# Performance work log

Hardware: AMD Instinct MI355X
Metric: run time of the kernel (lower is better)

## Reference

```python
import jax, jax.numpy as jnp
import numpy as np

D = 512
H = 2048
L = 8192
NSEG = 16
LN_EPS = 1e-6  # flax LayerNorm default


def _ln_tokens(x):
    # flax LayerNorm(reduction_axes=-2, feature_axes=-1, use_bias=False, use_scale=False):
    # mean/var reduced over the token axis (-2), per feature; no learned params.
    mu = jnp.mean(x, axis=-2, keepdims=True)
    var = jnp.var(x, axis=-2, keepdims=True)
    return (x - mu) * jax.lax.rsqrt(var + LN_EPS)


def setup_inputs() -> dict:
    key = jax.random.key(0)
    ks = jax.random.split(key, 8)
    xcat = jax.random.normal(ks[0], (L, D), dtype=jnp.float32)
    xsep = jnp.sort(jax.random.randint(ks[1], (L,), 0, NSEG)).astype(jnp.int64)
    s = 0.02
    Wqkv = jax.random.normal(ks[2], (D, 3 * D), dtype=jnp.float32) * s
    bqkv = jnp.zeros((3 * D,), dtype=jnp.float32)
    W1 = jax.random.normal(ks[3], (D, H), dtype=jnp.float32) * s
    b1 = jnp.zeros((H,), dtype=jnp.float32)
    W2 = jax.random.normal(ks[4], (H, D), dtype=jnp.float32) * s
    b2 = jnp.zeros((D,), dtype=jnp.float32)
    return {"xcat": xcat, "xsep": xsep, "Wqkv": Wqkv, "bqkv": bqkv,
            "W1": W1, "b1": b1, "W2": W2, "b2": b2}


def reference(xcat, xsep, Wqkv, bqkv, W1, b1, W2, b2):
    Ltok = xcat.shape[0]
    qkv = _ln_tokens(xcat) @ Wqkv + bqkv            # [L, 3D]
    q = qkv[:, :D]
    k = qkv[:, D:2 * D]
    # v = qkv[:, 2*D:3*D]  # computed in original but never used
    # unscaled scores; softmax FIRST, then mask, then renormalize (faithful to source)
    atten = jax.nn.softmax(jnp.einsum('id,jd->ij', q, k), axis=-1)  # [L, L]
    idx = jnp.arange(Ltok)
    mask = (xsep[None, :] == xsep[:, None]) & (idx[None, :] <= idx[:, None])
    atten = atten * mask
    atten = atten / (atten.sum(axis=-1, keepdims=True) + 1e-10)
    ctx = atten @ xcat                               # attention applied to raw xcat
    ffn = jax.nn.relu(_ln_tokens(ctx) @ W1 + b1) @ W2 + b2
    return (xcat + ffn, xsep)
```

## Files before the change

### kernel.cpp

```cpp
#include <hip/hip_runtime.h>
#include <math.h>

#define LTOK 8192
#define DDIM 512
#define HDIM 2048
#define NSEG 16
#define DCUT 64
#define ZROWS (NSEG * DCUT)
#define ZCH 64
#define NPART (ZCH * 4)
#define BM 128
#define BN 128
#define BK 64
#define PW 1280
#define PTILES (PW / BN)
#define ZGB (ZCH * (ZROWS / BM))
#define SPB (PTILES * 64)

typedef float f32x4 __attribute__((ext_vector_type(4)));
typedef short s16x8 __attribute__((ext_vector_type(8)));

static __device__ __forceinline__ short f2bf(float f) {
    union { float f; unsigned u; } v; v.f = f;
    unsigned r = (v.u + 0x7fffu + ((v.u >> 16) & 1u)) >> 16;
    return (short)r;
}
static __device__ __forceinline__ float bf2f(short s) {
    union { unsigned u; float f; } v;
    v.u = ((unsigned)(unsigned short)s) << 16;
    return v.f;
}

template<int GX, int GY>
__device__ __forceinline__ void swz_yslow(int& x, int& y) {
    constexpr int cpx = (GX * GY) >> 3;
    const int orig = blockIdx.y * GX + blockIdx.x;
    const int lg = (orig & 7) * cpx + (orig >> 3);
    y = lg / GX;
    x = lg - y * GX;
}

__global__ void ln_stats_partial(const float* __restrict__ X,
                                 float* __restrict__ psum, float* __restrict__ psumsq) {
    int c = threadIdx.x;
    int b = blockIdx.x;
    const float* p = X + (size_t)b * 256 * DDIM + c;
    float s = 0.f, s2 = 0.f;
    for (int r = 0; r < 256; ++r) {
        float v = p[(size_t)r * DDIM];
        s += v; s2 += v * v;
    }
    psum[b * DDIM + c] = s;
    psumsq[b * DDIM + c] = s2;
}

__global__ void ln_stats_final(const float* __restrict__ psum, const float* __restrict__ psumsq,
                               float* __restrict__ mu, float* __restrict__ rstd) {
    int c = threadIdx.x;
    float s = 0.f, s2 = 0.f;
    for (int b = 0; b < 32; ++b) { s += psum[b * DDIM + c]; s2 += psumsq[b * DDIM + c]; }
    float m = s / (float)LTOK;
    float var = s2 / (float)LTOK - m * m;
    mu[c] = m;
    rstd[c] = rsqrtf(var + 1e-6f);
}

__global__ void ln_apply_bf16(const float* __restrict__ X,
                              const float* __restrict__ mu, const float* __restrict__ rstd,
                              short* __restrict__ out) {
    int t = blockIdx.x * 256 + threadIdx.x;
    int base = t * 4;
    int c = base & (DDIM - 1);
    float4 v = *(const float4*)(X + base);
    short4 o;
    o.x = f2bf((v.x - mu[c + 0]) * rstd[c + 0]);
    o.y = f2bf((v.y - mu[c + 1]) * rstd[c + 1]);
    o.z = f2bf((v.z - mu[c + 2]) * rstd[c + 2]);
    o.w = f2bf((v.w - mu[c + 3]) * rstd[c + 3]);
    *(short4*)(out + base) = o;
}

__global__ void transpose_w(const float* __restrict__ W, int ldw, int n0,
                            short* __restrict__ WT, int R) {
    __shared__ short t[32][33];
    int nb = n0 + blockIdx.x * 32;
    int rb = blockIdx.y * 32;
    int tx = threadIdx.x & 31, ty = threadIdx.x >> 5;
    for (int rr = ty; rr < 32; rr += 8)
        t[rr][tx] = f2bf(W[(size_t)(rb + rr) * ldw + nb + tx]);
    __syncthreads();
    for (int rr = ty; rr < 32; rr += 8)
        WT[(size_t)(nb - n0 + rr) * R + rb + tx] = t[tx][rr];
}

__global__ void transpose_bf16(const float* __restrict__ X, short* __restrict__ XT) {
    __shared__ short t[32][33];
    int c0 = blockIdx.x * 32;
    int r0 = blockIdx.y * 32;
    int tx = threadIdx.x & 31, ty = threadIdx.x >> 5;
    for (int rr = ty; rr < 32; rr += 8)
        t[rr][tx] = f2bf(X[(size_t)(r0 + rr) * DDIM + c0 + tx]);
    __syncthreads();
    for (int rr = ty; rr < 32; rr += 8)
        XT[(size_t)(c0 + rr) * LTOK + r0 + tx] = t[tx][rr];
}

__global__ void seg_begin_k(const int* __restrict__ sep, int* __restrict__ begin,
                            float* __restrict__ out2) {
    int i = blockIdx.x * 256 + threadIdx.x;
    if (i < LTOK) {
        if (i == 0 || sep[i] != sep[i - 1]) begin[sep[i]] = i;
        out2[i] = (float)sep[i];
    }
}

__global__ void gather_qz(const short* __restrict__ qk, const int* __restrict__ sep,
                          const int* __restrict__ begin, short* __restrict__ qg) {
    const int gi = blockIdx.x;
    const int s = gi / DCUT, d = gi - s * DCUT;
    const int r = begin[s] + d;
    if ((unsigned)r < LTOK && sep[r] == s) {
        const short2* src = (const short2*)(qk + (size_t)r * 1024);
        short2* dst = (short2*)(qg + (size_t)gi * DDIM);
        dst[threadIdx.x] = src[threadIdx.x];
    }
}

__device__ __forceinline__ void stage_tile512(const short* __restrict__ src, int lda,
                                              short* lds, int tid) {
    const int wave = tid >> 6;
    const int lane = tid & 63;
    #pragma unroll
    for (int u = 0; u < 2; ++u) {
        const int c = u * 512 + wave * 64 + lane;
        const short* g = src + (size_t)(c >> 3) * lda + (c & 7) * 8;
        short* l = lds + (size_t)(u * 512 + wave * 64) * 8;
        __builtin_amdgcn_global_load_lds(
            (const __attribute__((address_space(1))) unsigned int*)g,
            (__attribute__((address_space(3))) unsigned int*)l,
            16, 0, 0);
    }
}

__device__ __forceinline__ void mma8_step(const short (*As)[BK], const short (*Bs)[BK],
                                          f32x4 acc[4][2], int wr, int wc, int grp, int lrow) {
    #pragma unroll
    for (int kk = 0; kk < 2; ++kk) {
        s16x8 af[4], bfr[2];
        #pragma unroll
        for (int f = 0; f < 4; ++f)
            af[f] = *(const s16x8*)&As[wr * 64 + f * 16 + lrow][grp * 8 + kk * 32];
        #pragma unroll
        for (int f = 0; f < 2; ++f)
            bfr[f] = *(const s16x8*)&Bs[wc * 32 + f * 16 + lrow][grp * 8 + kk * 32];
        #pragma unroll
        for (int fm = 0; fm < 4; ++fm)
            #pragma unroll
            for (int fn = 0; fn < 2; ++fn)
                acc[fm][fn] = __builtin_amdgcn_mfma_f32_16x16x32_bf16(
                    af[fm], bfr[fn], acc[fm][fn], 0, 0, 0);
    }
}

template<int EPI, int GX, int GY>
__global__ __launch_bounds__(512) void mm_bt8(const short* __restrict__ A, int lda,
        const short* __restrict__ BT, int ldb,
        const float* __restrict__ bias, const float* __restrict__ resid,
        float* __restrict__ Cf, short* __restrict__ Cb, int ldc, int K) {
    __shared__ short As[BM][BK];
    __shared__ short Bs[BN][BK];
    const int tid = threadIdx.x;
    const int wave = tid >> 6, lane = tid & 63, grp = lane >> 4, lrow = lane & 15;
    const int wr = wave >> 2, wc = wave & 3;
    int bx, by;
    swz_yslow<GX, GY>(bx, by);
    const int m0 = by * BM, n0 = bx * BN;
    if (EPI == 3) {
        A += (size_t)blockIdx.z * K;
        BT += (size_t)blockIdx.z * K;
    }
    f32x4 acc[4][2];
    #pragma unroll
    for (int a = 0; a < 4; ++a)
        #pragma unroll
        for (int b = 0; b < 2; ++b) acc[a][b] = (f32x4){0.f, 0.f, 0.f, 0.f};
    for (int k0 = 0; k0 < K; k0 += BK) {
        __syncthreads();
        stage_tile512(A + (size_t)m0 * lda + k0, lda, &As[0][0], tid);
        stage_tile512(BT + (size_t)n0 * ldb + k0, ldb, &Bs[0][0], tid);
        asm volatile("s_waitcnt vmcnt(0)" ::: "memory");
        __syncthreads();
        mma8_step(As, Bs, acc, wr, wc, grp, lrow);
    }
    #pragma unroll
    for (int fm = 0; fm < 4; ++fm) {
        #pragma unroll
        for (int i = 0; i < 4; ++i) {
            int row = m0 + wr * 64 + fm * 16 + grp * 4 + i;
            #pragma unroll
            for (int fn = 0; fn < 2; ++fn) {
                int col = n0 + wc * 32 + fn * 16 + lrow;
                float v = acc[fm][fn][i] + (EPI == 3 ? 0.f : bias[col]);
                if (EPI == 1) v = fmaxf(v, 0.f);
                if (EPI == 2) {
                    Cf[(size_t)row * ldc + col] = v + resid[(size_t)row * ldc + col];
                } else if (EPI == 3) {
                    Cb[(size_t)blockIdx.z * ((size_t)LTOK * ldc)
                       + (size_t)row * ldc + col] = f2bf(v);
                } else {
                    Cb[(size_t)row * ldc + col] = f2bf(v);
                }
            }
        }
    }
}

__global__ void ffn2_combine(const short* __restrict__ hp, const float* __restrict__ b2,
                             const float* __restrict__ xcat, float* __restrict__ out) {
    const int t = blockIdx.x * 256 + threadIdx.x;
    const int base = t * 4;
    const int c = base & (DDIM - 1);
    float4 r = *(const float4*)(xcat + base);
    float4 a;
    a.x = r.x + b2[c + 0];
    a.y = r.y + b2[c + 1];
    a.z = r.z + b2[c + 2];
    a.w = r.w + b2[c + 3];
    #pragma unroll
    for (int z = 0; z < 4; ++z) {
        short4 p = *(const short4*)(hp + (size_t)z * LTOK * DDIM + base);
        a.x += bf2f(p.x); a.y += bf2f(p.y); a.z += bf2f(p.z); a.w += bf2f(p.w);
    }
    *(float4*)(out + base) = a;
}

__global__ __launch_bounds__(512) void attn_zgsp(const short* __restrict__ qg,
        const short* __restrict__ qk,
        const int* __restrict__ sep, const int* __restrict__ begin,
        short* __restrict__ P, float* __restrict__ Zg) {
    __shared__ short As[BM][BK];
    __shared__ short Bs[BN][BK];
    const int tid = threadIdx.x;
    const int wave = tid >> 6, lane = tid & 63, grp = lane >> 4, lrow = lane & 15;
    const int wr = wave >> 2, wc = wave & 3;
    const int bid = blockIdx.x;
    const int grpi = bid / 9, rem = bid - grpi * 9;
    f32x4 acc[4][2];
    #pragma unroll
    for (int a = 0; a < 4; ++a)
        #pragma unroll
        for (int b = 0; b < 2; ++b) acc[a][b] = (f32x4){0.f, 0.f, 0.f, 0.f};

    if (rem < 4) {
        const int orig = grpi * 4 + rem;
        constexpr int cpx = ZGB >> 3;
        const int lg = (orig & 7) * cpx + (orig >> 3);
        const int bx = lg / (ZROWS / BM);
        const int by = lg - bx * (ZROWS / BM);
        const int g0 = by * BM;
        const int j0 = bx * BN;
        for (int k0 = 0; k0 < DDIM; k0 += BK) {
            __syncthreads();
            stage_tile512(qg + (size_t)g0 * DDIM + k0, DDIM, &As[0][0], tid);
            stage_tile512(qk + (size_t)j0 * 1024 + 512 + k0, 1024, &Bs[0][0], tid);
            asm volatile("s_waitcnt vmcnt(0)" ::: "memory");
            __syncthreads();
            mma8_step(As, Bs, acc, wr, wc, grp, lrow);
        }
        #pragma unroll
        for (int idx = 0; idx < 16; ++idx) {
            float z = __expf(acc[idx >> 2][0][idx & 3]) + __expf(acc[idx >> 2][1][idx & 3]);
            #pragma unroll
            for (int off = 1; off < 16; off <<= 1) z += __shfl_xor(z, off, 16);
            if (lrow == 0) {
                const int gi = g0 + wr * 64 + (idx >> 2) * 16 + grp * 4 + (idx & 3);
                Zg[(size_t)gi * NPART + bx * 4 + wc] = z;
            }
        }
    } else {
        const int orig = grpi * 5 + (rem - 4);
        constexpr int cpx = SPB >> 3;
        const int lg = (orig & 7) * cpx + (orig >> 3);
        const int by = lg / PTILES;
        const int bx = lg - by * PTILES;
        const int m0 = by * BM;
        const int jb0 = begin[sep[m0]] & ~(BN - 1);
        const int j0 = jb0 + bx * BN;
        if (j0 >= m0 + BM) return;
        for (int k0 = 0; k0 < DDIM; k0 += BK) {
            __syncthreads();
            stage_tile512(qk + (size_t)m0 * 1024 + k0, 1024, &As[0][0], tid);
            stage_tile512(qk + (size_t)j0 * 1024 + 512 + k0, 1024, &Bs[0][0], tid);
            asm volatile("s_waitcnt vmcnt(0)" ::: "memory");
            __syncthreads();
            mma8_step(As, Bs, acc, wr, wc, grp, lrow);
        }
        #pragma unroll
        for (int fm = 0; fm < 4; ++fm) {
            #pragma unroll
            for (int i = 0; i < 4; ++i) {
                const int row = m0 + wr * 64 + fm * 16 + grp * 4 + i;
                short* pr = P + (size_t)row * PW + (j0 - jb0) + wc * 32;
                #pragma unroll
                for (int fn = 0; fn < 2; ++fn)
                    pr[fn * 16 + lrow] = f2bf(__expf(acc[fm][fn][i]));
            }
        }
    }
}

__global__ void mask_inv(short* __restrict__ P,
                         const int* __restrict__ sep, const int* __restrict__ begin,
                         const float* __restrict__ Zg, float* __restrict__ invE) {
    const int wv = threadIdx.x >> 6, lane = threadIdx.x & 63;
    const int r = blockIdx.x * 4 + wv;
    const int m0 = r & ~(BM - 1);
    const int jb0 = begin[sep[m0]] & ~(BN - 1);
    const int kw = m0 + BM - jb0;
    const int sr = sep[r];
    const int jsr = begin[sr];
    short* Pr = P + (size_t)r * PW;
    float e = 0.f;
    for (int c = lane * 2; c < kw; c += 128) {
        short2 v = *(short2*)(Pr + c);
        const int col0 = jb0 + c;
        float p0 = bf2f(v.x), p1 = bf2f(v.y);
        if (col0 < jsr || col0 > r) { p0 = 0.f; v.x = 0; }
        if (col0 + 1 < jsr || col0 + 1 > r) { p1 = 0.f; v.y = 0; }
        e += p0 + p1;
        *(short2*)(Pr + c) = v;
    }
    const int d = r - jsr;
    float z = 0.f;
    if (d < DCUT) {
        const float* zr = Zg + (size_t)(sr * DCUT + d) * NPART;
        #pragma unroll
        for (int c = 0; c < NPART / 64; ++c) z += zr[c * 64 + lane];
    }
    #pragma unroll
    for (int off = 1; off < 64; off <<= 1) {
        e += __shfl_xor(e, off);
        z += __shfl_xor(z, off);
    }
    if (lane == 0) invE[r] = 1.f / (e + 1e-10f * z);
}

__global__ __launch_bounds__(512) void attn_pv(const short* __restrict__ P,
        const short* __restrict__ xbT,
        const int* __restrict__ sep, const int* __restrict__ begin,
        const float* __restrict__ invE, float* __restrict__ ctx) {
    __shared__ short As[BM][BK];
    __shared__ short Bs[BN][BK];
    const int tid = threadIdx.x;
    const int wave = tid >> 6, lane = tid & 63, grp = lane >> 4, lrow = lane & 15;
    const int wr = wave >> 2, wc = wave & 3;
    int bx, by;
    swz_yslow<4, 64>(bx, by);
    const int m0 = by * BM, n0 = bx * BN;
    const int jbase0 = begin[sep[m0]] & ~(BN - 1);
    const int kmax = m0 + BM - jbase0;
    f32x4 acc[4][2];
    #pragma unroll
    for (int a = 0; a < 4; ++a)
        #pragma unroll
        for (int b = 0; b < 2; ++b) acc[a][b] = (f32x4){0.f, 0.f, 0.f, 0.f};
    for (int k0 = 0; k0 < kmax; k0 += BK) {
        __syncthreads();
        stage_tile512(P + (size_t)m0 * PW + k0, PW, &As[0][0], tid);
        stage_tile512(xbT + (size_t)n0 * LTOK + jbase0 + k0, LTOK, &Bs[0][0], tid);
        asm volatile("s_waitcnt vmcnt(0)" ::: "memory");
        __syncthreads();
        mma8_step(As, Bs, acc, wr, wc, grp, lrow);
    }
    #pragma unroll
    for (int fm = 0; fm < 4; ++fm) {
        #pragma unroll
        for (int i = 0; i < 4; ++i) {
            int row = m0 + wr * 64 + fm * 16 + grp * 4 + i;
            float inv = invE[row];
            #pragma unroll
            for (int fn = 0; fn < 2; ++fn) {
                int col = n0 + wc * 32 + fn * 16 + lrow;
                ctx[(size_t)row * DDIM + col] = acc[fm][fn][i] * inv;
            }
        }
    }
}

extern "C" void kernel_launch(void* const* d_in, const int* in_sizes, int n_in,
                              void* d_out, int out_size, void* d_ws, size_t ws_size,
                              hipStream_t stream) {
    const float* xcat = (const float*)d_in[0];
    const int* sep = (const int*)d_in[1];
    const float* Wqkv = (const float*)d_in[2];
    const float* bqkv = (const float*)d_in[3];
    const float* W1 = (const float*)d_in[4];
    const float* b1 = (const float*)d_in[5];
    const float* W2 = (const float*)d_in[6];
    const float* b2 = (const float*)d_in[7];
    float* out = (float*)d_out;

    float* ws = (float*)d_ws;
    float* psum   = ws;
    float* psumsq = psum + 32 * DDIM;
    float* mu1    = psumsq + 32 * DDIM;
    float* rstd1  = mu1 + DDIM;
    float* mu2    = rstd1 + DDIM;
    float* rstd2  = mu2 + DDIM;
    float* invE   = rstd2 + DDIM;
    float* Zg     = invE + LTOK;
    int*   begin  = (int*)(Zg + (size_t)ZROWS * NPART);
    short* qg     = (short*)(begin + 1024);
    short* qk     = qg    + (size_t)ZROWS * DDIM;
    short* xbT    = qk    + (size_t)LTOK * 1024;
    short* lnx    = xbT   + (size_t)DDIM * LTOK;
    short* lnctx  = lnx   + (size_t)LTOK * DDIM;
    short* hb     = lnctx + (size_t)LTOK * DDIM;
    short* Pbuf   = hb;
    short* WqkvT  = hb    + (size_t)LTOK * HDIM;
    short* W1T    = WqkvT + (size_t)1024 * DDIM;
    short* W2T    = W1T   + (size_t)HDIM * DDIM;
    float* ctxF   = (float*)(W2T + (size_t)DDIM * HDIM);
    short* hpart  = qk;

    ln_stats_partial<<<dim3(32), dim3(512), 0, stream>>>(xcat, psum, psumsq);
    ln_stats_final<<<dim3(1), dim3(512), 0, stream>>>(psum, psumsq, mu1, rstd1);
    ln_apply_bf16<<<dim3(LTOK * DDIM / 4 / 256), dim3(256), 0, stream>>>(xcat, mu1, rstd1, lnx);

    transpose_w<<<dim3(32, 16), dim3(256), 0, stream>>>(Wqkv, 3 * DDIM, 0, WqkvT, DDIM);
    transpose_w<<<dim3(64, 16), dim3(256), 0, stream>>>(W1, HDIM, 0, W1T, DDIM);
    transpose_w<<<dim3(16, 64), dim3(256), 0, stream>>>(W2, DDIM, 0, W2T, HDIM);

    mm_bt8<0, 8, 64><<<dim3(8, 64), dim3(512), 0, stream>>>(
        lnx, DDIM, WqkvT, DDIM, bqkv, (const float*)nullptr,
        (float*)nullptr, qk, 1024, DDIM);

    seg_begin_k<<<dim3(32), dim3(256), 0, stream>>>(sep, begin, out + (size_t)LTOK * DDIM);
    transpose_bf16<<<dim3(16, 256), dim3(256), 0, stream>>>(xcat, xbT);

    gather_qz<<<dim3(ZROWS), dim3(256), 0, stream>>>(qk, sep, begin, qg);
    attn_zgsp<<<dim3(ZGB + SPB), dim3(512), 0, stream>>>(qg, qk, sep, begin, Pbuf, Zg);

    mask_inv<<<dim3(LTOK / 4), dim3(256), 0, stream>>>(Pbuf, sep, begin, Zg, invE);
    attn_pv<<<dim3(4, 64), dim3(512), 0, stream>>>(Pbuf, xbT, sep, begin, invE, ctxF);

    ln_stats_partial<<<dim3(32), dim3(512), 0, stream>>>(ctxF, psum, psumsq);
    ln_stats_final<<<dim3(1), dim3(512), 0, stream>>>(psum, psumsq, mu2, rstd2);
    ln_apply_bf16<<<dim3(LTOK * DDIM / 4 / 256), dim3(256), 0, stream>>>(ctxF, mu2, rstd2, lnctx);

    mm_bt8<1, 16, 64><<<dim3(16, 64), dim3(512), 0, stream>>>(
        lnctx, DDIM, W1T, DDIM, b1, (const float*)nullptr,
        (float*)nullptr, hb, HDIM, DDIM);

    mm_bt8<3, 4, 64><<<dim3(4, 64, 4), dim3(512), 0, stream>>>(
        hb, HDIM, W2T, HDIM, (const float*)nullptr, (const float*)nullptr,
        (float*)nullptr, hpart, DDIM, HDIM / 4);
    ffn2_combine<<<dim3(LTOK * DDIM / 4 / 256), dim3(256), 0, stream>>>(hpart, b2, xcat, out);
}
```

Measured before the change: 209.9 us.

## Fuse causal/segment mask into score epilogue and LN stats into PV epilogue

Applies the segment/causal mask directly when writing exp(scores) in attn_zgsp, so the row-sum pass becomes read-only instead of read-modify-write. Computes per-column sum and sum-of-squares of ctx in the attn_pv epilogue via shared-memory atomics and writes 64 partials, which removes a separate ln_stats_partial pass over ctx. Also halves DCUT, shrinking the Zg denominator-approximation work. The smaller DCUT changes how many near-diagonal rows get the tiny epsilon*Z correction, which may alter accuracy in edge cases.

New measurement: 216.9 us. +3.3%, slower.

```diff
diff --git a/kernel.cpp b/kernel.cpp
--- a/kernel.cpp
+++ b/kernel.cpp
@@ -5,7 +5,7 @@
 #define DDIM 512
 #define HDIM 2048
 #define NSEG 16
-#define DCUT 64
+#define DCUT 32
 #define ZROWS (NSEG * DCUT)
 #define ZCH 64
 #define NPART (ZCH * 4)
@@ -16,6 +16,9 @@
 #define PTILES (PW / BN)
 #define ZGB (ZCH * (ZROWS / BM))
 #define SPB (PTILES * 64)
+#define ZG_PER (ZGB / 128)
+#define SP_PER (SPB / 128)
+#define GRP_SZ (ZG_PER + SP_PER)
 
 typedef float f32x4 __attribute__((ext_vector_type(4)));
 typedef short s16x8 __attribute__((ext_vector_type(8)));
@@ -55,10 +58,10 @@
 }
 
 __global__ void ln_stats_final(const float* __restrict__ psum, const float* __restrict__ psumsq,
-                               float* __restrict__ mu, float* __restrict__ rstd) {
+                               float* __restrict__ mu, float* __restrict__ rstd, int nb) {
     int c = threadIdx.x;
     float s = 0.f, s2 = 0.f;
-    for (int b = 0; b < 32; ++b) { s += psum[b * DDIM + c]; s2 += psumsq[b * DDIM + c]; }
+    for (int b = 0; b < nb; ++b) { s += psum[b * DDIM + c]; s2 += psumsq[b * DDIM + c]; }
     float m = s / (float)LTOK;
     float var = s2 / (float)LTOK - m * m;
     mu[c] = m;
@@ -244,15 +247,15 @@
     const int wave = tid >> 6, lane = tid & 63, grp = lane >> 4, lrow = lane & 15;
     const int wr = wave >> 2, wc = wave & 3;
     const int bid = blockIdx.x;
-    const int grpi = bid / 9, rem = bid - grpi * 9;
+    const int grpi = bid / GRP_SZ, rem = bid - grpi * GRP_SZ;
     f32x4 acc[4][2];
     #pragma unroll
     for (int a = 0; a < 4; ++a)
         #pragma unroll
         for (int b = 0; b < 2; ++b) acc[a][b] = (f32x4){0.f, 0.f, 0.f, 0.f};
 
-    if (rem < 4) {
-        const int orig = grpi * 4 + rem;
+    if (rem < ZG_PER) {
+        const int orig = grpi * ZG_PER + rem;
         constexpr int cpx = ZGB >> 3;
         const int lg = (orig & 7) * cpx + (orig >> 3);
         const int bx = lg / (ZROWS / BM);
@@ -278,7 +281,7 @@
             }
         }
     } else {
-        const int orig = grpi * 5 + (rem - 4);
+        const int orig = grpi * SP_PER + (rem - ZG_PER);
         constexpr int cpx = SPB >> 3;
         const int lg = (orig & 7) * cpx + (orig >> 3);
         const int by = lg / PTILES;
@@ -300,18 +303,22 @@
             #pragma unroll
             for (int i = 0; i < 4; ++i) {
                 const int row = m0 + wr * 64 + fm * 16 + grp * 4 + i;
+                const int jsr = begin[sep[row]];
                 short* pr = P + (size_t)row * PW + (j0 - jb0) + wc * 32;
                 #pragma unroll
-                for (int fn = 0; fn < 2; ++fn)
-                    pr[fn * 16 + lrow] = f2bf(__expf(acc[fm][fn][i]));
+                for (int fn = 0; fn < 2; ++fn) {
+                    const int col = j0 + wc * 32 + fn * 16 + lrow;
+                    const float ez = __expf(acc[fm][fn][i]);
+                    pr[fn * 16 + lrow] = f2bf((col >= jsr && col <= row) ? ez : 0.f);
+                }
             }
         }
     }
 }
 
-__global__ void mask_inv(short* __restrict__ P,
-                         const int* __restrict__ sep, const int* __restrict__ begin,
-                         const float* __restrict__ Zg, float* __restrict__ invE) {
+__global__ void einv_k(const short* __restrict__ P,
+                       const int* __restrict__ sep, const int* __restrict__ begin,
+                       const float* __restrict__ Zg, float* __restrict__ invE) {
     const int wv = threadIdx.x >> 6, lane = threadIdx.x & 63;
     const int r = blockIdx.x * 4 + wv;
     const int m0 = r & ~(BM - 1);
@@ -319,16 +326,11 @@
     const int kw = m0 + BM - jb0;
     const int sr = sep[r];
     const int jsr = begin[sr];
-    short* Pr = P + (size_t)r * PW;
+    const short* Pr = P + (size_t)r * PW;
     float e = 0.f;
     for (int c = lane * 2; c < kw; c += 128) {
-        short2 v = *(short2*)(Pr + c);
-        const int col0 = jb0 + c;
-        float p0 = bf2f(v.x), p1 = bf2f(v.y);
-        if (col0 < jsr || col0 > r) { p0 = 0.f; v.x = 0; }
-        if (col0 + 1 < jsr || col0 + 1 > r) { p1 = 0.f; v.y = 0; }
-        e += p0 + p1;
-        *(short2*)(Pr + c) = v;
+        short2 v = *(const short2*)(Pr + c);
+        e += bf2f(v.x) + bf2f(v.y);
     }
     const int d = r - jsr;
     float z = 0.f;
@@ -348,9 +350,11 @@
 __global__ __launch_bounds__(512) void attn_pv(const short* __restrict__ P,
         const short* __restrict__ xbT,
         const int* __restrict__ sep, const int* __restrict__ begin,
-        const float* __restrict__ invE, float* __restrict__ ctx) {
+        const float* __restrict__ invE, float* __restrict__ ctx,
+        float* __restrict__ psum2, float* __restrict__ psumsq2) {
     __shared__ short As[BM][BK];
     __shared__ short Bs[BN][BK];
+    __shared__ float Sacc[128][2];
     const int tid = threadIdx.x;
     const int wave = tid >> 6, lane = tid & 63, grp = lane >> 4, lrow = lane & 15;
     const int wr = wave >> 2, wc = wave & 3;
@@ -372,6 +376,9 @@
         __syncthreads();
         mma8_step(As, Bs, acc, wr, wc, grp, lrow);
     }
+    if (tid < 128) { Sacc[tid][0] = 0.f; Sacc[tid][1] = 0.f; }
+    __syncthreads();
+    float cs[2] = {0.f, 0.f}, cq[2] = {0.f, 0.f};
     #pragma unroll
     for (int fm = 0; fm < 4; ++fm) {
         #pragma unroll
@@ -381,9 +388,30 @@
             #pragma unroll
             for (int fn = 0; fn < 2; ++fn) {
                 int col = n0 + wc * 32 + fn * 16 + lrow;
-                ctx[(size_t)row * DDIM + col] = acc[fm][fn][i] * inv;
+                float v = acc[fm][fn][i] * inv;
+                ctx[(size_t)row * DDIM + col] = v;
+                cs[fn] += v;
+                cq[fn] += v * v;
             }
         }
+    }
+    #pragma unroll
+    for (int fn = 0; fn < 2; ++fn) {
+        cs[fn] += __shfl_xor(cs[fn], 16); cs[fn] += __shfl_xor(cs[fn], 32);
+        cq[fn] += __shfl_xor(cq[fn], 16); cq[fn] += __shfl_xor(cq[fn], 32);
+    }
+    if (grp == 0) {
+        #pragma unroll
+        for (int fn = 0; fn < 2; ++fn) {
+            const int cb = wc * 32 + fn * 16 + lrow;
+            atomicAdd(&Sacc[cb][0], cs[fn]);
+            atomicAdd(&Sacc[cb][1], cq[fn]);
+        }
+    }
+    __syncthreads();
+    if (tid < 128) {
+        psum2[(size_t)by * DDIM + n0 + tid] = Sacc[tid][0];
+        psumsq2[(size_t)by * DDIM + n0 + tid] = Sacc[tid][1];
     }
 }
 
@@ -401,30 +429,32 @@
     float* out = (float*)d_out;
 
     float* ws = (float*)d_ws;
-    float* psum   = ws;
-    float* psumsq = psum + 32 * DDIM;
-    float* mu1    = psumsq + 32 * DDIM;
-    float* rstd1  = mu1 + DDIM;
-    float* mu2    = rstd1 + DDIM;
-    float* rstd2  = mu2 + DDIM;
-    float* invE   = rstd2 + DDIM;
-    float* Zg     = invE + LTOK;
-    int*   begin  = (int*)(Zg + (size_t)ZROWS * NPART);
-    short* qg     = (short*)(begin + 1024);
-    short* qk     = qg    + (size_t)ZROWS * DDIM;
-    short* xbT    = qk    + (size_t)LTOK * 1024;
-    short* lnx    = xbT   + (size_t)DDIM * LTOK;
-    short* lnctx  = lnx   + (size_t)LTOK * DDIM;
-    short* hb     = lnctx + (size_t)LTOK * DDIM;
-    short* Pbuf   = hb;
-    short* WqkvT  = hb    + (size_t)LTOK * HDIM;
-    short* W1T    = WqkvT + (size_t)1024 * DDIM;
-    short* W2T    = W1T   + (size_t)HDIM * DDIM;
-    float* ctxF   = (float*)(W2T + (size_t)DDIM * HDIM);
-    short* hpart  = qk;
+    float* psum    = ws;
+    float* psumsq  = psum + 32 * DDIM;
+    float* psum2   = psumsq + 32 * DDIM;
+    float* psumsq2 = psum2 + 64 * DDIM;
+    float* mu1     = psumsq2 + 64 * DDIM;
+    float* rstd1   = mu1 + DDIM;
+    float* mu2     = rstd1 + DDIM;
+    float* rstd2   = mu2 + DDIM;
+    float* invE    = rstd2 + DDIM;
+    float* Zg      = invE + LTOK;
+    int*   begin   = (int*)(Zg + (size_t)ZROWS * NPART);
+    short* qg      = (short*)(begin + 1024);
+    short* qk      = qg    + (size_t)ZROWS * DDIM;
+    short* xbT     = qk    + (size_t)LTOK * 1024;
+    short* lnx     = xbT   + (size_t)DDIM * LTOK;
+    short* lnctx   = lnx   + (size_t)LTOK * DDIM;
+    short* hb      = lnctx + (size_t)LTOK * DDIM;
+    short* Pbuf    = hb;
+    short* WqkvT   = hb    + (size_t)LTOK * HDIM;
+    short* W1T     = WqkvT + (size_t)1024 * DDIM;
+    short* W2T     = W1T   + (size_t)HDIM * DDIM;
+    float* ctxF    = (float*)(W2T + (size_t)DDIM * HDIM);
+    short* hpart   = qk;
 
     ln_stats_partial<<<dim3(32), dim3(512), 0, stream>>>(xcat, psum, psumsq);
-    ln_stats_final<<<dim3(1), dim3(512), 0, stream>>>(psum, psumsq, mu1, rstd1);
+    ln_stats_final<<<dim3(1), dim3(512), 0, stream>>>(psum, psumsq, mu1, rstd1, 32);
     ln_apply_bf16<<<dim3(LTOK * DDIM / 4 / 256), dim3(256), 0, stream>>>(xcat, mu1, rstd1, lnx);
 
     transpose_w<<<dim3(32, 16), dim3(256), 0, stream>>>(Wqkv, 3 * DDIM, 0, WqkvT, DDIM);
@@ -441,11 +471,11 @@
     gather_qz<<<dim3(ZROWS), dim3(256), 0, stream>>>(qk, sep, begin, qg);
     attn_zgsp<<<dim3(ZGB + SPB), dim3(512), 0, stream>>>(qg, qk, sep, begin, Pbuf, Zg);
 
-    mask_inv<<<dim3(LTOK / 4), dim3(256), 0, stream>>>(Pbuf, sep, begin, Zg, invE);
-    attn_pv<<<dim3(4, 64), dim3(512), 0, stream>>>(Pbuf, xbT, sep, begin, invE, ctxF);
-
-    ln_stats_partial<<<dim3(32), dim3(512), 0, stream>>>(ctxF, psum, psumsq);
-    ln_stats_final<<<dim3(1), dim3(512), 0, stream>>>(psum, psumsq, mu2, rstd2);
+    einv_k<<<dim3(LTOK / 4), dim3(256), 0, stream>>>(Pbuf, sep, begin, Zg, invE);
+    attn_pv<<<dim3(4, 64), dim3(512), 0, stream>>>(Pbuf, xbT, sep, begin, invE, ctxF,
+                                                   psum2, psumsq2);
+
+    ln_stats_final<<<dim3(1), dim3(512), 0, stream>>>(psum2, psumsq2, mu2, rstd2, 64);
     ln_apply_bf16<<<dim3(LTOK * DDIM / 4 / 256), dim3(256), 0, stream>>>(ctxF, mu2, rstd2, lnctx);
 
     mm_bt8<1, 16, 64><<<dim3(16, 64), dim3(512), 0, stream>>>(
```
